# Performance work log

Measured on AMD Instinct MI355X. Metric: run time of the kernel, lower is better.

Reference implementation:

```python
import jax, jax.numpy as jnp
import numpy as np
jax.config.update("jax_enable_x64", True)

R = 8192          # num_reqs
SPEC = 7          # draft tokens per request
T = 1 + SPEC      # tokens emitted per request next step
SC = SPEC + 1     # sampled_cols (verified positions)
MAX_BLOCKS = 2048
BLOCK_SIZE = 128
VOCAB = 152064
NUM_PHYS_BLOCKS = 1 << 20


def setup_inputs() -> dict:
    key = jax.random.key(0)
    k = jax.random.split(key, 8)
    base = jax.random.randint(k[0], (R,), 0, 200000, dtype=jnp.int64)
    # positions of the previous step's T input tokens are consecutive per request
    input_positions = (base[:, None] + jnp.arange(T, dtype=jnp.int64)).reshape(-1)
    return {
        "input_tokens": jax.random.randint(k[1], (R * T,), 0, VOCAB, dtype=jnp.int64),
        "sampled_tokens": jax.random.randint(k[2], (R, SC), 0, VOCAB, dtype=jnp.int64),
        "input_positions": input_positions,
        "seq_lens": base + T,
        "slot_mapping": jax.random.randint(k[3], (R * T,), 0, NUM_PHYS_BLOCKS * BLOCK_SIZE, dtype=jnp.int64),
        "block_table": jax.random.randint(k[4], (R, MAX_BLOCKS), 0, NUM_PHYS_BLOCKS, dtype=jnp.int64),
        "spec_tokens": jax.random.randint(k[5], (R, SPEC), 0, VOCAB, dtype=jnp.int64),
        "accepted_num": jax.random.randint(k[6], (R,), 1, SC + 1, dtype=jnp.int64),
        "num_seqs": R,
        "num_queries": R,
        "block_size": BLOCK_SIZE,
    }


def reference(input_tokens, sampled_tokens, input_positions, seq_lens, slot_mapping,
              block_table, spec_tokens, accepted_num, num_seqs, num_queries, block_size):
    num_reqs = num_seqs
    spec_num = spec_tokens.shape[1]
    t = 1 + spec_num                      # tokens per request
    sc = sampled_tokens.shape[1]
    a = jnp.clip(accepted_num, 1, sc)     # accepted length in [1, sc]
    # position of previous step's first input token, per request
    prev_base = input_positions.reshape(num_reqs, t)[:, 0]
    base = prev_base + a                  # position of new first token [R]
    pos = base[:, None] + jnp.arange(t, dtype=pos_dtype(base))  # [R, T]
    # token 0: last accepted sampled token; tokens 1..: new draft tokens
    first = jnp.take_along_axis(sampled_tokens, (a - 1)[:, None], axis=1)  # [R,1]
    out_tokens = jnp.concatenate([first, spec_tokens], axis=1)             # [R,T]
    # slot mapping via block table gather
    blk = jnp.take_along_axis(block_table, pos // block_size, axis=1)      # [R,T]
    slots = blk * block_size + pos % block_size
    out_seq_lens = pos + 1
    return (out_tokens.reshape(-1), pos.reshape(-1),
            out_seq_lens.reshape(-1), slots.reshape(-1))


def pos_dtype(x):
    return x.dtype
```

## Files before the change

### kernel.cpp

```cpp
#include <hip/hip_runtime.h>


__global__ __launch_bounds__(256) void spec_prep_kernel(
    const int* __restrict__ input_positions,
    const int* __restrict__ sampled_tokens,
    const int* __restrict__ block_table,
    const int* __restrict__ spec_tokens,
    const int* __restrict__ accepted_num,
    const int* __restrict__ block_size_p,
    int* __restrict__ out,
    int T, int SC, int SPEC, int MAXB, int N)
{
    int idx = blockIdx.x * blockDim.x + threadIdx.x;
    if (idx >= N) return;

    int r = idx / T;
    int j = idx - r * T;

    int bs = *block_size_p;

    int a = accepted_num[r];
    a = a < 1 ? 1 : (a > SC ? SC : a);

    int prev_base = input_positions[r * T];
    int pos = prev_base + a + j;

    int tok = (j == 0) ? sampled_tokens[r * SC + (a - 1)]
                       : spec_tokens[r * SPEC + (j - 1)];

    int blk = block_table[r * MAXB + pos / bs];
    int slot = blk * bs + pos % bs;

    out[idx]         = tok;
    out[N + idx]     = pos;
    out[2 * N + idx] = pos + 1;
    out[3 * N + idx] = slot;
}

extern "C" void kernel_launch(void* const* d_in, const int* in_sizes, int n_in,
                              void* d_out, int out_size, void* d_ws, size_t ws_size,
                              hipStream_t stream) {
    const int* sampled_tokens  = (const int*)d_in[1];
    const int* input_positions = (const int*)d_in[2];
    const int* block_table     = (const int*)d_in[5];
    const int* spec_tokens     = (const int*)d_in[6];
    const int* accepted_num    = (const int*)d_in[7];
    const int* block_size_p    = (const int*)d_in[10];

    const int R    = in_sizes[7];
    const int N    = in_sizes[2];
    const int T    = N / R;
    const int SC   = in_sizes[1] / R;
    const int SPEC = in_sizes[6] / R;
    const int MAXB = in_sizes[5] / R;

    int* out = (int*)d_out;

    const int block = 256;
    const int grid = (N + block - 1) / block;
    spec_prep_kernel<<<grid, block, 0, stream>>>(
        input_positions, sampled_tokens, block_table, spec_tokens,
        accepted_num, block_size_p, out, T, SC, SPEC, MAXB, N);
}
```

Before: 109.2 us.

## Process one request per thread with vectorized int4 stores for T=8

Adds a specialized kernel for T=8 and SPEC=7 that assigns one request per thread instead of one token per thread. It loads the per-request scalars once, fetches at most two block-table entries, and writes each output row as two int4 stores. This is meant to cut redundant loads and scalar stores. In exchange there are fewer threads, with 8192 total, which may hurt latency hiding on the scattered block_table gathers. The spec_tokens reads per thread are strided rather than coalesced.

Result: no change. 109.0 us (-0.2%).

```diff
diff --git a/kernel.cpp b/kernel.cpp
--- a/kernel.cpp
+++ b/kernel.cpp
@@ -1,7 +1,63 @@
 #include <hip/hip_runtime.h>
 
 
-__global__ __launch_bounds__(256) void spec_prep_kernel(
+__global__ __launch_bounds__(256) void spec_prep_t8_kernel(
+    const int* __restrict__ input_positions,
+    const int* __restrict__ sampled_tokens,
+    const int* __restrict__ block_table,
+    const int* __restrict__ spec_tokens,
+    const int* __restrict__ accepted_num,
+    const int* __restrict__ block_size_p,
+    int* __restrict__ out,
+    int SC, int MAXB, int R, int N)
+{
+    int r = blockIdx.x * blockDim.x + threadIdx.x;
+    if (r >= R) return;
+
+    const int bs = *block_size_p;
+
+    int a = accepted_num[r];
+    a = a < 1 ? 1 : (a > SC ? SC : a);
+
+    const int base = input_positions[r * 8] + a;
+
+    int tok[8];
+    tok[0] = sampled_tokens[r * SC + (a - 1)];
+    const int* sp = spec_tokens + r * 7;
+    #pragma unroll
+    for (int j = 0; j < 7; ++j) tok[j + 1] = sp[j];
+
+    const int d0 = base / bs;
+    const int d7 = (base + 7) / bs;
+    const int* btr = block_table + (long)r * MAXB;
+    const int b0 = btr[d0];
+    const int b1 = (d7 == d0) ? b0 : btr[d7];
+
+    int pos[8], slot[8];
+    #pragma unroll
+    for (int j = 0; j < 8; ++j) {
+        pos[j] = base + j;
+        const int d = pos[j] / bs;
+        const int blk = (d == d0) ? b0 : b1;
+        slot[j] = blk * bs + (pos[j] - d * bs);
+    }
+
+    int4* o_tok  = (int4*)(out) + r * 2;
+    int4* o_pos  = (int4*)(out + N) + r * 2;
+    int4* o_seq  = (int4*)(out + 2 * N) + r * 2;
+    int4* o_slot = (int4*)(out + 3 * N) + r * 2;
+
+    o_tok[0]  = make_int4(tok[0], tok[1], tok[2], tok[3]);
+    o_tok[1]  = make_int4(tok[4], tok[5], tok[6], tok[7]);
+    o_pos[0]  = make_int4(pos[0], pos[1], pos[2], pos[3]);
+    o_pos[1]  = make_int4(pos[4], pos[5], pos[6], pos[7]);
+    o_seq[0]  = make_int4(pos[0] + 1, pos[1] + 1, pos[2] + 1, pos[3] + 1);
+    o_seq[1]  = make_int4(pos[4] + 1, pos[5] + 1, pos[6] + 1, pos[7] + 1);
+    o_slot[0] = make_int4(slot[0], slot[1], slot[2], slot[3]);
+    o_slot[1] = make_int4(slot[4], slot[5], slot[6], slot[7]);
+}
+
+__global__ __launch_bounds__(256) void spec_prep_generic_kernel(
     const int* __restrict__ input_positions,
     const int* __restrict__ sampled_tokens,
     const int* __restrict__ block_table,
@@ -13,28 +69,19 @@
 {
     int idx = blockIdx.x * blockDim.x + threadIdx.x;
     if (idx >= N) return;
-
     int r = idx / T;
     int j = idx - r * T;
-
     int bs = *block_size_p;
-
     int a = accepted_num[r];
     a = a < 1 ? 1 : (a > SC ? SC : a);
-
-    int prev_base = input_positions[r * T];
-    int pos = prev_base + a + j;
-
+    int pos = input_positions[r * T] + a + j;
     int tok = (j == 0) ? sampled_tokens[r * SC + (a - 1)]
                        : spec_tokens[r * SPEC + (j - 1)];
-
-    int blk = block_table[r * MAXB + pos / bs];
-    int slot = blk * bs + pos % bs;
-
+    int blk = block_table[(long)r * MAXB + pos / bs];
     out[idx]         = tok;
     out[N + idx]     = pos;
     out[2 * N + idx] = pos + 1;
-    out[3 * N + idx] = slot;
+    out[3 * N + idx] = blk * bs + pos % bs;
 }
 
 extern "C" void kernel_launch(void* const* d_in, const int* in_sizes, int n_in,
@@ -56,9 +103,17 @@
 
     int* out = (int*)d_out;
 
-    const int block = 256;
-    const int grid = (N + block - 1) / block;
-    spec_prep_kernel<<<grid, block, 0, stream>>>(
-        input_positions, sampled_tokens, block_table, spec_tokens,
-        accepted_num, block_size_p, out, T, SC, SPEC, MAXB, N);
+    if (T == 8 && SPEC == 7) {
+        const int block = 256;
+        const int grid = (R + block - 1) / block;
+        spec_prep_t8_kernel<<<grid, block, 0, stream>>>(
+            input_positions, sampled_tokens, block_table, spec_tokens,
+            accepted_num, block_size_p, out, SC, MAXB, R, N);
+    } else {
+        const int block = 256;
+        const int grid = (N + block - 1) / block;
+        spec_prep_generic_kernel<<<grid, block, 0, stream>>>(
+            input_positions, sampled_tokens, block_table, spec_tokens,
+            accepted_num, block_size_p, out, T, SC, SPEC, MAXB, N);
+    }
 }
```
